# Kernel tuning notes

Measured on AMD Instinct MI355X. Metric: run time of the kernel, lower is better.

The kernel has to match this reference:

```python
import jax, jax.numpy as jnp
import numpy as np

D_MODEL = 1024
NUM_HEADS = 16
D_K = D_MODEL // NUM_HEADS


def setup_inputs() -> dict:
    key = jax.random.key(0)
    ks = jax.random.split(key, 9)
    s = 1.0 / np.sqrt(D_MODEL)
    x = jax.random.normal(ks[0], (1, 4096, D_MODEL), dtype=jnp.float32)
    Wq = jax.random.uniform(ks[1], (D_MODEL, D_MODEL), jnp.float32, -s, s)
    bq = jax.random.uniform(ks[2], (D_MODEL,), jnp.float32, -s, s)
    Wk = jax.random.uniform(ks[3], (D_MODEL, D_MODEL), jnp.float32, -s, s)
    bk = jax.random.uniform(ks[4], (D_MODEL,), jnp.float32, -s, s)
    Wv = jax.random.uniform(ks[5], (D_MODEL, D_MODEL), jnp.float32, -s, s)
    bv = jax.random.uniform(ks[6], (D_MODEL,), jnp.float32, -s, s)
    Wo = jax.random.uniform(ks[7], (D_MODEL, D_MODEL), jnp.float32, -s, s)
    bo = jax.random.uniform(ks[8], (D_MODEL,), jnp.float32, -s, s)
    return {"x": x, "Wq": Wq, "bq": bq, "Wk": Wk, "bk": bk,
            "Wv": Wv, "bv": bv, "Wo": Wo, "bo": bo}


def reference(x, Wq, bq, Wk, bk, Wv, bv, Wo, bo):
    B, S, _ = x.shape
    scale = jnp.sqrt(jnp.asarray(D_K, dtype=x.dtype))
    # projections (torch Linear: y = x @ W.T + b)
    q = (x @ Wq.T + bq).reshape(B, S, NUM_HEADS, D_K).transpose(0, 2, 1, 3)
    k = (x @ Wk.T + bk).reshape(B, S, NUM_HEADS, D_K).transpose(0, 2, 1, 3)
    v = (x @ Wv.T + bv).reshape(B, S, NUM_HEADS, D_K).transpose(0, 2, 1, 3)
    # [B, H, S, S] naive scores, causal mask, softmax
    scores = jnp.einsum('bhqd,bhkd->bhqk', q, k) / scale
    causal = jnp.tril(jnp.ones((S, S), dtype=bool))
    scores = jnp.where(causal, scores, jnp.asarray(-jnp.inf, dtype=scores.dtype))
    probs = jax.nn.softmax(scores, axis=-1)
    out = jnp.einsum('bhqk,bhkd->bhqd', probs, v)
    out = out.transpose(0, 2, 1, 3).reshape(B, S, D_MODEL)
    return out @ Wo.T + bo
```

## Files before the change

kernel.cpp:

```cpp
#include <hip/hip_runtime.h>
#include <math.h>

#define SEQ 4096
#define DMODEL 1024
#define NH 16
#define DK 64
#define LDP 72

typedef __bf16    bf16x8 __attribute__((ext_vector_type(8)));
typedef float     f32x4  __attribute__((ext_vector_type(4)));
typedef __fp16    fp16x2 __attribute__((ext_vector_type(2)));
typedef _Float16  h16x2  __attribute__((ext_vector_type(2)));
typedef _Float16  h16x4  __attribute__((ext_vector_type(4)));
typedef _Float16  h16x8  __attribute__((ext_vector_type(8)));

#define GLOAD_LDS16(g, l) __builtin_amdgcn_global_load_lds(                     \
    (const __attribute__((address_space(1))) unsigned int*)(g),                 \
    (__attribute__((address_space(3))) unsigned int*)(l), 16, 0, 0)

__device__ __forceinline__ h16x2 cvt_pk_h16(float a, float b) {
    fp16x2 r = __builtin_amdgcn_cvt_pkrtz(a, b);
    return __builtin_bit_cast(h16x2, r);
}

#define EXP2R(x) __builtin_amdgcn_exp2f(x)

__global__ __launch_bounds__(256)
void cvt_all(const float* __restrict__ x, const float* __restrict__ Wq,
             const float* __restrict__ Wk, const float* __restrict__ Wv,
             const float* __restrict__ Wo, __bf16* __restrict__ dst)
{
    const size_t M1 = 1u << 20;
    const size_t e = ((size_t)blockIdx.x * 256 + threadIdx.x) * 8;
    const float* src; size_t off;
    if      (e < 4*M1) { src = x;  off = e;        }
    else if (e < 5*M1) { src = Wq; off = e - 4*M1; }
    else if (e < 6*M1) { src = Wk; off = e - 5*M1; }
    else if (e < 7*M1) { src = Wv; off = e - 6*M1; }
    else               { src = Wo; off = e - 7*M1; }
    const float4 f0 = *reinterpret_cast<const float4*>(&src[off]);
    const float4 f1 = *reinterpret_cast<const float4*>(&src[off + 4]);
    bf16x8 pk;
    pk[0]=(__bf16)f0.x; pk[1]=(__bf16)f0.y; pk[2]=(__bf16)f0.z; pk[3]=(__bf16)f0.w;
    pk[4]=(__bf16)f1.x; pk[5]=(__bf16)f1.y; pk[6]=(__bf16)f1.z; pk[7]=(__bf16)f1.w;
    *reinterpret_cast<bf16x8*>(&dst[e]) = pk;
}

__device__ __forceinline__ void gemm_core64(const __bf16* __restrict__ A,
                                            const __bf16* __restrict__ W,
                                            int m0, int n0, int t,
                                            __bf16* AsF, __bf16* BsF,
                                            f32x4 acc[2][4])
{
    const int w = t >> 6, lane = t & 63, l15 = lane & 15, quad = lane >> 4;
    const int lr = lane >> 3, lc = lane & 7;
    for (int k0 = 0; k0 < DMODEL; k0 += 64) {
        __syncthreads();
        #pragma unroll
        for (int p = 0; p < 4; ++p) {
            const int n = w*4 + p;
            const int r = n*8 + lr;
            const int cl = lc ^ (r & 7);
            GLOAD_LDS16(&A[(size_t)(m0 + r) * DMODEL + k0 + cl*8], &AsF[n*512]);
        }
        #pragma unroll
        for (int p = 0; p < 2; ++p) {
            const int n = w*2 + p;
            const int r = n*8 + lr;
            const int cl = lc ^ (r & 7);
            GLOAD_LDS16(&W[(size_t)(n0 + r) * DMODEL + k0 + cl*8], &BsF[n*512]);
        }
        __syncthreads();
        #pragma unroll
        for (int kb = 0; kb < 2; ++kb) {
            const int phys = ((kb*4 + quad) ^ (l15 & 7)) * 8;
            bf16x8 af0 = *reinterpret_cast<const bf16x8*>(&AsF[(w*32 + l15)*64 + phys]);
            bf16x8 af1 = *reinterpret_cast<const bf16x8*>(&AsF[(w*32 + 16 + l15)*64 + phys]);
            #pragma unroll
            for (int ns = 0; ns < 4; ++ns) {
                const bf16x8 bfr = *reinterpret_cast<const bf16x8*>(&BsF[(ns*16 + l15)*64 + phys]);
                acc[0][ns] = __builtin_amdgcn_mfma_f32_16x16x32_bf16(af0, bfr, acc[0][ns], 0, 0, 0);
                acc[1][ns] = __builtin_amdgcn_mfma_f32_16x16x32_bf16(af1, bfr, acc[1][ns], 0, 0, 0);
            }
        }
    }
}

__global__ __launch_bounds__(256, 6)
void gemm_qkv(const __bf16* __restrict__ xb, const __bf16* __restrict__ Wcat,
              const float* __restrict__ bq, const float* __restrict__ bk,
              const float* __restrict__ bv,
              _Float16* __restrict__ Qh, _Float16* __restrict__ Kh, _Float16* __restrict__ Vth)
{
    __shared__ __bf16 SM[12288];
    __bf16* AsF = SM;
    __bf16* BsF = SM + 8192;
    const int t = threadIdx.x;
    const int n0g = blockIdx.x * 64;
    const int m0  = blockIdx.y * 128;
    const int which = n0g >> 10;
    const int n_in  = n0g & 1023;

    f32x4 acc[2][4] = {};
    gemm_core64(xb, Wcat, m0, n0g, t, AsF, BsF, acc);

    const int w = t >> 6, lane = t & 63, l15 = lane & 15, quad = lane >> 4;
    const float* bias = (which == 0) ? bq : (which == 1) ? bk : bv;
    float br[4];
    #pragma unroll
    for (int ns = 0; ns < 4; ++ns) br[ns] = bias[n_in + ns*16 + l15];

    if (which == 2) {
        #pragma unroll
        for (int ms = 0; ms < 2; ++ms)
            #pragma unroll
            for (int ns = 0; ns < 4; ++ns) {
                h16x4 pk;
                #pragma unroll
                for (int rg = 0; rg < 4; ++rg) pk[rg] = (_Float16)(acc[ms][ns][rg] + br[ns]);
                *reinterpret_cast<h16x4*>(
                    &Vth[(size_t)(n_in + ns*16 + l15) * SEQ + m0 + w*32 + ms*16 + quad*4]) = pk;
            }
    } else {
        const float s = (which == 0) ? 0.1803368787f : 1.0f;
        _Float16* C = (which == 0) ? Qh : Kh;
        __syncthreads();
        _Float16* tile = (_Float16*)SM + w * 32 * LDP;
        #pragma unroll
        for (int ms = 0; ms < 2; ++ms)
            #pragma unroll
            for (int ns = 0; ns < 4; ++ns)
                #pragma unroll
                for (int rg = 0; rg < 4; ++rg)
                    tile[(ms*16 + quad*4 + rg) * LDP + ns*16 + l15] =
                        (_Float16)((acc[ms][ns][rg] + br[ns]) * s);
        asm volatile("s_waitcnt lgkmcnt(0)" ::: "memory");
        const int er = lane >> 3, ec = (lane & 7) * 8;
        #pragma unroll
        for (int p = 0; p < 4; ++p) {
            const h16x8 v = *reinterpret_cast<const h16x8*>(&tile[(er + p*8) * LDP + ec]);
            *reinterpret_cast<h16x8*>(
                &C[(size_t)(m0 + w*32 + er + p*8) * DMODEL + n_in + ec]) = v;
        }
    }
}

__global__ __launch_bounds__(256, 4)
void gemm_out(const __bf16* __restrict__ Ob, const __bf16* __restrict__ Wob,
              const float* __restrict__ bo, float* __restrict__ out)
{
    __shared__ __bf16 AsF[64*64];
    __shared__ __bf16 BsF[64*64];
    const int t = threadIdx.x;
    const int n0 = blockIdx.x * 64;
    const int m0 = blockIdx.y * 64;
    const int w = t >> 6, lane = t & 63, l15 = lane & 15, quad = lane >> 4;
    const int lr = lane >> 3, lc = lane & 7;

    f32x4 acc[4] = {};
    for (int k0 = 0; k0 < DMODEL; k0 += 64) {
        __syncthreads();
        #pragma unroll
        for (int p = 0; p < 2; ++p) {
            const int n = w*2 + p;
            const int r = n*8 + lr;
            const int cl = lc ^ (r & 7);
            GLOAD_LDS16(&Ob [(size_t)(m0 + r) * DMODEL + k0 + cl*8], &AsF[n*512]);
            GLOAD_LDS16(&Wob[(size_t)(n0 + r) * DMODEL + k0 + cl*8], &BsF[n*512]);
        }
        __syncthreads();
        #pragma unroll
        for (int kb = 0; kb < 2; ++kb) {
            const int phys = ((kb*4 + quad) ^ (l15 & 7)) * 8;
            const bf16x8 af = *reinterpret_cast<const bf16x8*>(&AsF[(w*16 + l15)*64 + phys]);
            #pragma unroll
            for (int ns = 0; ns < 4; ++ns) {
                const bf16x8 bfr = *reinterpret_cast<const bf16x8*>(&BsF[(ns*16 + l15)*64 + phys]);
                acc[ns] = __builtin_amdgcn_mfma_f32_16x16x32_bf16(af, bfr, acc[ns], 0, 0, 0);
            }
        }
    }

    float br[4];
    #pragma unroll
    for (int ns = 0; ns < 4; ++ns) br[ns] = bo[n0 + ns*16 + l15];
    #pragma unroll
    for (int ns = 0; ns < 4; ++ns)
        #pragma unroll
        for (int rg = 0; rg < 4; ++rg)
            out[(size_t)(m0 + w*16 + quad*4 + rg) * DMODEL + n0 + ns*16 + l15] =
                acc[ns][rg] + br[ns];
}

__global__ __launch_bounds__(256, 3)
void attn_mfma(const _Float16* __restrict__ Q, const _Float16* __restrict__ K,
               const _Float16* __restrict__ Vt, __bf16* __restrict__ O,
               _Float16* __restrict__ partA, _Float16* __restrict__ partB,
               float* __restrict__ lpart)
{
    __shared__ _Float16 KsF[2][64*64];
    __shared__ _Float16 VsF[2][64*64];

    const int t = threadIdx.x;
    const int w = t >> 6;
    const int lane = t & 63, l15 = lane & 15, quad = lane >> 4;
    const int lr = lane >> 3, lc = lane & 7;
    const int h = blockIdx.y;
    const int u = blockIdx.x;

    const int cl = lc ^ lr;
    const int rA = (w*2 + 0)*8 + lr, rB = (w*2 + 1)*8 + lr;
    const int dA = (w*2 + 0)*512,   dB = (w*2 + 1)*512;
    const h16x4 vone = {(_Float16)1.f, (_Float16)1.f, (_Float16)1.f, (_Float16)1.f};

    int g = u * 22;
    const int gend = g + 22;
    int qt = 0;
    while ((qt + 1) * (qt + 2) <= g) ++qt;

    while (g < gend) {
        const int S = qt * (qt + 1);
        const int rowlen = 2*qt + 2;
        const int ts = g - S;
        const int rem = gend - S;
        const int te = (rowlen < rem) ? rowlen : rem;
        const int s0 = qt*128 + w*16;
        const int s1 = s0 + 64;

        h16x8 bq8[2][2];
        #pragma unroll
        for (int kb = 0; kb < 2; ++kb) {
            bq8[0][kb] = *reinterpret_cast<const h16x8*>(
                &Q[(size_t)(s0 + l15) * DMODEL + h*DK + kb*32 + quad*8]);
            bq8[1][kb] = *reinterpret_cast<const h16x8*>(
                &Q[(size_t)(s1 + l15) * DMODEL + h*DK + kb*32 + quad*8]);
        }

        const _Float16* kpA = &K [(size_t)(ts*64 + rA) * DMODEL + h*DK + cl*8];
        const _Float16* kpB = &K [(size_t)(ts*64 + rB) * DMODEL + h*DK + cl*8];
        const _Float16* vpA = &Vt[(size_t)(h*DK + rA) * SEQ + ts*64 + cl*8];
        const _Float16* vpB = &Vt[(size_t)(h*DK + rB) * SEQ + ts*64 + cl*8];

#define STAGE_KV(bi) do {                                     \
        GLOAD_LDS16(kpA, &KsF[bi][dA]);                       \
        GLOAD_LDS16(kpB, &KsF[bi][dB]);                       \
        GLOAD_LDS16(vpA, &VsF[bi][dA]);                       \
        GLOAD_LDS16(vpB, &VsF[bi][dB]);                       \
        kpA += (size_t)64*DMODEL; kpB += (size_t)64*DMODEL;   \
        vpA += 64; vpB += 64; } while (0)

        f32x4 acc[2][4] = {};
        f32x4 accl[2] = {};

        STAGE_KV(0);
        __syncthreads();

        int pbuf = 0;
        for (int tk = ts; tk < te; ++tk, pbuf ^= 1) {
            if (tk + 1 < te) STAGE_KV(pbuf ^ 1);

            const int j0 = tk * 64;
            const bool act0 = (j0 <= s0 + 15);
            const bool msk0 = (j0 + 63 > s0);
            const bool msk1 = (j0 + 63 > s1);
            const int rel0 = s0 - j0 + l15;
            const int rel1 = s1 - j0 + l15;

            h16x4 ap[2][4];
            #pragma unroll
            for (int st = 0; st < 4; ++st) {
                const h16x8 ak0 = *reinterpret_cast<const h16x8*>(
                    &KsF[pbuf][(st*16 + l15)*64 + ((quad ^ (l15 & 7)))*8]);
                const h16x8 ak1 = *reinterpret_cast<const h16x8*>(
                    &KsF[pbuf][(st*16 + l15)*64 + (((4 + quad) ^ (l15 & 7)))*8]);
                {
                    f32x4 cc = {0.f, 0.f, 0.f, 0.f};
                    cc = __builtin_amdgcn_mfma_f32_16x16x32_f16(ak0, bq8[1][0], cc, 0, 0, 0);
                    cc = __builtin_amdgcn_mfma_f32_16x16x32_f16(ak1, bq8[1][1], cc, 0, 0, 0);
                    float pv[4];
                    if (msk1) {
                        #pragma unroll
                        for (int rg = 0; rg < 4; ++rg) {
                            const float e = EXP2R(cc[rg]);
                            pv[rg] = (st*16 + quad*4 + rg > rel1) ? 0.f : e;
                        }
                    } else {
                        #pragma unroll
                        for (int rg = 0; rg < 4; ++rg) pv[rg] = EXP2R(cc[rg]);
                    }
                    const h16x2 lo = cvt_pk_h16(pv[0], pv[1]);
                    const h16x2 hi = cvt_pk_h16(pv[2], pv[3]);
                    ap[1][st] = (h16x4){lo[0], lo[1], hi[0], hi[1]};
                    accl[1] = __builtin_amdgcn_mfma_f32_16x16x16f16(ap[1][st], vone, accl[1], 0, 0, 0);
                }
                if (act0) {
                    f32x4 cc = {0.f, 0.f, 0.f, 0.f};
                    cc = __builtin_amdgcn_mfma_f32_16x16x32_f16(ak0, bq8[0][0], cc, 0, 0, 0);
                    cc = __builtin_amdgcn_mfma_f32_16x16x32_f16(ak1, bq8[0][1], cc, 0, 0, 0);
                    float pv[4];
                    if (msk0) {
                        #pragma unroll
                        for (int rg = 0; rg < 4; ++rg) {
                            const float e = EXP2R(cc[rg]);
                            pv[rg] = (st*16 + quad*4 + rg > rel0) ? 0.f : e;
                        }
                    } else {
                        #pragma unroll
                        for (int rg = 0; rg < 4; ++rg) pv[rg] = EXP2R(cc[rg]);
                    }
                    const h16x2 lo = cvt_pk_h16(pv[0], pv[1]);
                    const h16x2 hi = cvt_pk_h16(pv[2], pv[3]);
                    ap[0][st] = (h16x4){lo[0], lo[1], hi[0], hi[1]};
                    accl[0] = __builtin_amdgcn_mfma_f32_16x16x16f16(ap[0][st], vone, accl[0], 0, 0, 0);
                }
            }

            #pragma unroll
            for (int ds_ = 0; ds_ < 4; ++ds_) {
                #pragma unroll
                for (int st = 0; st < 4; ++st) {
                    const h16x4 bv = *reinterpret_cast<const h16x4*>(
                        &VsF[pbuf][(ds_*16 + l15)*64 +
                                   (((st*2 + (quad >> 1)) ^ (l15 & 7)))*8 + (quad & 1)*4]);
                    acc[1][ds_] = __builtin_amdgcn_mfma_f32_16x16x16f16(ap[1][st], bv, acc[1][ds_], 0, 0, 0);
                    if (act0)
                        acc[0][ds_] = __builtin_amdgcn_mfma_f32_16x16x16f16(ap[0][st], bv, acc[0][ds_], 0, 0, 0);
                }
            }
            __syncthreads();
        }
#undef STAGE_KV

        if (ts == 0 && te == rowlen) {
            #pragma unroll
            for (int s = 0; s < 2; ++s) {
                const int base = s ? s1 : s0;
                #pragma unroll
                for (int rg = 0; rg < 4; ++rg) {
                    const float inv = 1.0f / accl[s][rg];
                    const size_t row = (size_t)(base + quad*4 + rg) * DMODEL + h * DK;
                    #pragma unroll
                    for (int ds_ = 0; ds_ < 4; ++ds_)
                        O[row + ds_*16 + l15] = (__bf16)(acc[s][ds_][rg] * inv);
                }
            }
        } else {
            const int side = (g == u*22) ? 0 : 1;
            const int slot = (h*48 + u)*2 + side;
            _Float16* p = (slot < 1024) ? partA + (size_t)slot * 8192
                                        : partB + (size_t)(slot - 1024) * 8192;
            #pragma unroll
            for (int s = 0; s < 2; ++s) {
                #pragma unroll
                for (int rg = 0; rg < 4; ++rg) {
                    const int lrow = s*64 + w*16 + quad*4 + rg;
                    #pragma unroll
                    for (int ds_ = 0; ds_ < 4; ++ds_)
                        p[lrow*64 + ds_*16 + l15] = (_Float16)acc[s][ds_][rg];
                    if (l15 == 0) lpart[(size_t)slot*128 + lrow] = accl[s][rg];
                }
            }
        }
        g = S + te;
        ++qt;
    }
}

__global__ __launch_bounds__(256)
void attn_combine(const _Float16* __restrict__ partA, const _Float16* __restrict__ partB,
                  const float* __restrict__ lpart, __bf16* __restrict__ O)
{
    const int t = threadIdx.x;
    const int qt = blockIdx.x;
    const int h  = blockIdx.y;
    const int S = qt*(qt+1);
    const int rowlen = 2*qt + 2;
    const int c0 = S / 22;
    const int c1 = (S + rowlen - 1) / 22;
    if (c0 == c1) return;
    const int r  = t >> 1;
    const int d0 = (t & 1) * 32;

    float a[4][8] = {};
    float l = 0.f;
    for (int c = c0; c <= c1; ++c) {
        const int side = (22*c >= S) ? 0 : 1;
        const int sl = (h*48 + c)*2 + side;
        const _Float16* pc = (sl < 1024) ? partA + (size_t)sl * 8192
                                         : partB + (size_t)(sl - 1024) * 8192;
        l += lpart[(size_t)sl*128 + r];
        #pragma unroll
        for (int i = 0; i < 4; ++i) {
            const h16x8 v = *reinterpret_cast<const h16x8*>(&pc[r*64 + d0 + i*8]);
            #pragma unroll
            for (int j = 0; j < 8; ++j) a[i][j] += (float)v[j];
        }
    }
    const float inv = 1.0f / l;
    const size_t grow = (size_t)(qt*128 + r) * DMODEL + h*64 + d0;
    #pragma unroll
    for (int i = 0; i < 4; ++i) {
        bf16x8 pk;
        #pragma unroll
        for (int j = 0; j < 8; ++j) pk[j] = (__bf16)(a[i][j] * inv);
        *reinterpret_cast<bf16x8*>(&O[grow + i*8]) = pk;
    }
}

extern "C" void kernel_launch(void* const* d_in, const int* in_sizes, int n_in,
                              void* d_out, int out_size, void* d_ws, size_t ws_size,
                              hipStream_t stream) {
    const float* x  = (const float*)d_in[0];
    const float* Wq = (const float*)d_in[1];
    const float* bq = (const float*)d_in[2];
    const float* Wk = (const float*)d_in[3];
    const float* bk = (const float*)d_in[4];
    const float* Wv = (const float*)d_in[5];
    const float* bv = (const float*)d_in[6];
    const float* Wo = (const float*)d_in[7];
    const float* bo = (const float*)d_in[8];
    float* out = (float*)d_out;

    const size_t M1 = 1u << 20;
    __bf16* base = (__bf16*)d_ws;
    __bf16*    xb   = base;
    __bf16*    Wcat = base + 4*M1;
    __bf16*    Wob  = base + 7*M1;
    _Float16*  Qh   = (_Float16*)(base + 8*M1);
    _Float16*  Kh   = (_Float16*)(base + 12*M1);
    _Float16*  Vth  = (_Float16*)(base + 16*M1);
    __bf16*    Ob   = base + 20*M1;
    _Float16*  partA = (_Float16*)out;
    _Float16*  partB = (_Float16*)xb;
    float*     lpart = (float*)Wcat;

    cvt_all<<<4096, 256, 0, stream>>>(x, Wq, Wk, Wv, Wo, base);
    gemm_qkv<<<dim3(48, 32), 256, 0, stream>>>(xb, Wcat, bq, bk, bv, Qh, Kh, Vth);
    attn_mfma<<<dim3(48, NH), 256, 0, stream>>>(Qh, Kh, Vth, Ob, partA, partB, lpart);
    attn_combine<<<dim3(32, NH), 256, 0, stream>>>(partA, partB, lpart, Ob);
    gemm_out<<<dim3(16, 64), 256, 0, stream>>>(Ob, Wob, bo, out);
}
```

Baseline: 227.3 us.

## Swap QKV GEMM operand roles and remap attention blocks per XCD

Measured after the change: 212.1 us. -6.7%, faster.

```diff
diff --git a/kernel.cpp b/kernel.cpp
--- a/kernel.cpp
+++ b/kernel.cpp
@@ -92,55 +92,51 @@
               const float* __restrict__ bv,
               _Float16* __restrict__ Qh, _Float16* __restrict__ Kh, _Float16* __restrict__ Vth)
 {
-    __shared__ __bf16 SM[12288];
-    __bf16* AsF = SM;
-    __bf16* BsF = SM + 8192;
+    __shared__ __bf16 AsF[128*64];
+    __shared__ __bf16 BsF[64*64];
     const int t = threadIdx.x;
-    const int n0g = blockIdx.x * 64;
-    const int m0  = blockIdx.y * 128;
+    const int n0g = blockIdx.x * 128;
+    const int m0  = blockIdx.y * 64;
     const int which = n0g >> 10;
     const int n_in  = n0g & 1023;
 
     f32x4 acc[2][4] = {};
-    gemm_core64(xb, Wcat, m0, n0g, t, AsF, BsF, acc);
+    gemm_core64(Wcat, xb, n0g, m0, t, AsF, BsF, acc);
 
     const int w = t >> 6, lane = t & 63, l15 = lane & 15, quad = lane >> 4;
     const float* bias = (which == 0) ? bq : (which == 1) ? bk : bv;
-    float br[4];
+    float4 fb[2];
     #pragma unroll
-    for (int ns = 0; ns < 4; ++ns) br[ns] = bias[n_in + ns*16 + l15];
+    for (int ms = 0; ms < 2; ++ms)
+        fb[ms] = *reinterpret_cast<const float4*>(&bias[n_in + w*32 + ms*16 + quad*4]);
 
     if (which == 2) {
         #pragma unroll
-        for (int ms = 0; ms < 2; ++ms)
+        for (int ms = 0; ms < 2; ++ms) {
+            const float fb4[4] = {fb[ms].x, fb[ms].y, fb[ms].z, fb[ms].w};
+            #pragma unroll
+            for (int rg = 0; rg < 4; ++rg) {
+                const size_t row = (size_t)(n_in + w*32 + ms*16 + quad*4 + rg) * SEQ + m0;
+                #pragma unroll
+                for (int ns = 0; ns < 4; ++ns)
+                    Vth[row + ns*16 + l15] = (_Float16)(acc[ms][ns][rg] + fb4[rg]);
+            }
+        }
+    } else {
+        const float s = (which == 0) ? 0.1803368787f : 1.0f;
+        _Float16* C = (which == 0) ? Qh : Kh;
+        #pragma unroll
+        for (int ms = 0; ms < 2; ++ms) {
+            const float fb4[4] = {fb[ms].x, fb[ms].y, fb[ms].z, fb[ms].w};
             #pragma unroll
             for (int ns = 0; ns < 4; ++ns) {
                 h16x4 pk;
                 #pragma unroll
-                for (int rg = 0; rg < 4; ++rg) pk[rg] = (_Float16)(acc[ms][ns][rg] + br[ns]);
+                for (int rg = 0; rg < 4; ++rg)
+                    pk[rg] = (_Float16)((acc[ms][ns][rg] + fb4[rg]) * s);
                 *reinterpret_cast<h16x4*>(
-                    &Vth[(size_t)(n_in + ns*16 + l15) * SEQ + m0 + w*32 + ms*16 + quad*4]) = pk;
-            }
-    } else {
-        const float s = (which == 0) ? 0.1803368787f : 1.0f;
-        _Float16* C = (which == 0) ? Qh : Kh;
-        __syncthreads();
-        _Float16* tile = (_Float16*)SM + w * 32 * LDP;
-        #pragma unroll
-        for (int ms = 0; ms < 2; ++ms)
-            #pragma unroll
-            for (int ns = 0; ns < 4; ++ns)
-                #pragma unroll
-                for (int rg = 0; rg < 4; ++rg)
-                    tile[(ms*16 + quad*4 + rg) * LDP + ns*16 + l15] =
-                        (_Float16)((acc[ms][ns][rg] + br[ns]) * s);
-        asm volatile("s_waitcnt lgkmcnt(0)" ::: "memory");
-        const int er = lane >> 3, ec = (lane & 7) * 8;
-        #pragma unroll
-        for (int p = 0; p < 4; ++p) {
-            const h16x8 v = *reinterpret_cast<const h16x8*>(&tile[(er + p*8) * LDP + ec]);
-            *reinterpret_cast<h16x8*>(
-                &C[(size_t)(m0 + w*32 + er + p*8) * DMODEL + n_in + ec]) = v;
+                    &C[(size_t)(m0 + ns*16 + l15) * DMODEL + n_in + w*32 + ms*16 + quad*4]) = pk;
+            }
         }
     }
 }
@@ -205,8 +201,11 @@
     const int w = t >> 6;
     const int lane = t & 63, l15 = lane & 15, quad = lane >> 4;
     const int lr = lane >> 3, lc = lane & 7;
-    const int h = blockIdx.y;
-    const int u = blockIdx.x;
+    const int b = blockIdx.x;
+    const int xcd = b & 7;
+    const int j = b >> 3;
+    const int h = xcd*2 + (j >= 48 ? 1 : 0);
+    const int u = (j >= 48) ? j - 48 : j;
 
     const int cl = lc ^ lr;
     const int rA = (w*2 + 0)*8 + lr, rB = (w*2 + 1)*8 + lr;
@@ -435,8 +434,8 @@
     float*     lpart = (float*)Wcat;
 
     cvt_all<<<4096, 256, 0, stream>>>(x, Wq, Wk, Wv, Wo, base);
-    gemm_qkv<<<dim3(48, 32), 256, 0, stream>>>(xb, Wcat, bq, bk, bv, Qh, Kh, Vth);
-    attn_mfma<<<dim3(48, NH), 256, 0, stream>>>(Qh, Kh, Vth, Ob, partA, partB, lpart);
+    gemm_qkv<<<dim3(24, 64), 256, 0, stream>>>(xb, Wcat, bq, bk, bv, Qh, Kh, Vth);
+    attn_mfma<<<768, 256, 0, stream>>>(Qh, Kh, Vth, Ob, partA, partB, lpart);
     attn_combine<<<dim3(32, NH), 256, 0, stream>>>(partA, partB, lpart, Ob);
     gemm_out<<<dim3(16, 64), 256, 0, stream>>>(Ob, Wob, bo, out);
 }
```
